# Kernel optimization log

Measured on AMD Instinct MI355X. Metric: run time of the kernel, lower is better.

## Reference

```python
import jax, jax.numpy as jnp
import numpy as np

B, S, P, D = 4, 2, 1024, 1024   # batch, sample_count, seq (== n_ctx), d_embed
I, H = 16, 64                   # n_heads, d_head
ALPHA = 1.0                     # weight_alpha


def setup_inputs() -> dict:
    key = jax.random.key(0)
    kx, kk, kq, kv, ko = jax.random.split(key, 5)
    scale = ALPHA / np.sqrt(D)
    return {
        "x": jax.random.normal(kx, (B, S, P, D), dtype=jnp.float32),
        "W_K": (scale * jax.random.normal(kk, (S, I, H, D))).astype(jnp.float32),
        "W_Q": (scale * jax.random.normal(kq, (S, I, H, D))).astype(jnp.float32),
        "W_V": (scale * jax.random.normal(kv, (S, I, H, D))).astype(jnp.float32),
        "W_O": (scale * jax.random.normal(ko, (S, D, I * H))).astype(jnp.float32),
    }


def reference(x, W_K, W_Q, W_V, W_O):
    # x: [b, s, p, d]; W_{K,Q,V}: [s, i, h, d]; W_O: [s, d, i*h]
    k = jnp.einsum('sihd,bspd->bsiph', W_K, x)
    q = jnp.einsum('sihd,bspd->bsiph', W_Q, x)
    v = jnp.einsum('sihd,bspd->bsiph', W_V, x)
    # scores: [b, s, i, q, p] (query rows, key cols)
    scores = jnp.einsum('bsiph,bsiqh->bsiqp', k, q)
    p = x.shape[-2]
    mask = jnp.tril(jnp.ones((p, p), dtype=x.dtype))  # causal lower-triangular
    # faithful to torch: tril(scores) - 1e10 * (1 - mask), scaled AFTER masking
    masked = scores * mask - 1.0e10 * (1.0 - mask)
    attn = jax.nn.softmax(masked / np.sqrt(H), axis=-1)
    z = jnp.einsum('bsiph,bsiqp->bsiqh', v, attn)      # [b, s, i, q, h]
    b = x.shape[0]
    z_flat = jnp.transpose(z, (0, 1, 3, 2, 4)).reshape(b, S, p, I * H)  # b s q (i h)
    out = jnp.einsum('sdf,bsqf->bsqd', W_O, z_flat)
    return out
```

## Files before the change

kernel.cpp:

```cpp
#include <hip/hip_runtime.h>
#include <hip/hip_bf16.h>
#include <cmath>

#define C_B 4
#define C_S 2
#define C_P 1024
#define C_D 1024
#define C_I 16
#define C_H 64

typedef unsigned short u16;
typedef unsigned int u32;
typedef __attribute__((ext_vector_type(8))) short short8;
typedef __attribute__((ext_vector_type(8))) __bf16 bf16x8;
typedef __attribute__((ext_vector_type(4))) float f32x4;
typedef __attribute__((ext_vector_type(16))) float f32x16;
typedef __attribute__((ext_vector_type(4))) u32 u32x4;

__device__ __forceinline__ u16 f2bf(float f) {
  union { float f; unsigned u; } c; c.f = f;
  unsigned u = c.u;
  u += 0x7fffu + ((u >> 16) & 1u);
  return (u16)(u >> 16);
}

__device__ __forceinline__ u32 cvtpk_bf16(float lo, float hi) {
  u32 r;
  asm("v_cvt_pk_bf16_f32 %0, %1, %2" : "=v"(r) : "v"(lo), "v"(hi));
  return r;
}

__device__ __forceinline__ float fexp2(float x) {
  return __builtin_amdgcn_exp2f(x);
}

__device__ __forceinline__ f32x16 mfma32(short8 a, short8 b, f32x16 c) {
  return __builtin_amdgcn_mfma_f32_32x32x16_bf16(
      __builtin_bit_cast(bf16x8, a), __builtin_bit_cast(bf16x8, b), c, 0, 0, 0);
}

__device__ __forceinline__ void load_lds16(const u16* g, u16* l) {
  __builtin_amdgcn_global_load_lds(
      (const __attribute__((address_space(1))) void*)g,
      (__attribute__((address_space(3))) void*)l, 16, 0, 0);
}

__global__ void cvt_all(const float* __restrict__ x,
                        const float* __restrict__ wq, const float* __restrict__ wk,
                        const float* __restrict__ wvp, const float* __restrict__ wo,
                        u16* __restrict__ xbf, u16* __restrict__ wall,
                        u16* __restrict__ wob) {
  const int b = blockIdx.x;
  if (b < 2048) {
    int i = b * 256 + threadIdx.x;
    const int n4 = (C_B * C_S * C_P * C_D) / 4, stride = 2048 * 256;
    for (; i < n4; i += stride) {
      float4 v = reinterpret_cast<const float4*>(x)[i];
      ushort4 o;
      o.x = f2bf(v.x); o.y = f2bf(v.y); o.z = f2bf(v.z); o.w = f2bf(v.w);
      reinterpret_cast<ushort4*>(xbf)[i] = o;
    }
  } else {
    const int j = b - 2048;
    const int t = j >> 9;
    const float* src = (t == 0) ? wq : (t == 1) ? wk : (t == 2) ? wvp : wo;
    int i = (j & 511) * 256 + threadIdx.x;
    const int stride = 512 * 256;
    for (; i < 524288; i += stride) {
      float4 v = reinterpret_cast<const float4*>(src)[i];
      ushort4 o;
      o.x = f2bf(v.x); o.y = f2bf(v.y); o.z = f2bf(v.z); o.w = f2bf(v.w);
      if (t < 3) {
        int s = i >> 18;
        int rem = i & 262143;
        reinterpret_cast<ushort4*>(wall)[s * 786432 + t * 262144 + rem] = o;
      } else {
        reinterpret_cast<ushort4*>(wob)[i] = o;
      }
    }
  }
}

template<int MODE>
__global__ __launch_bounds__(512, 2)
void gemm_bt(const u16* __restrict__ A, const u16* __restrict__ Bm, void* __restrict__ C) {
  __shared__ __align__(16) u16 lds[49152];
  const int tid = threadIdx.x;
  const int lane = tid & 63;
  const int wv = tid >> 6;
  const int wr = wv >> 2, wc = wv & 3;
  const int l31 = lane & 31, l5 = lane >> 5;

  const int h = (int)blockIdx.x;
  const int lid = (MODE == 3) ? ((h & 7) * 96 + (h >> 3)) : ((h & 7) * 32 + (h >> 3));
  const int bs  = (MODE == 3) ? (lid / 96) : (lid >> 5);
  const int r2  = (MODE == 3) ? (lid % 96) : (lid & 31);
  const int bx = r2 & 7, by = r2 >> 3;
  const int m0 = bx * 128, n0 = by * 256;

  const u16* Ab = A + (size_t)bs * (C_P * C_D);
  const u16* Bb = Bm + (size_t)(bs & 1) * (MODE == 3 ? 3 * 1048576 : 1048576);
  f32x16 acc[2][2] = {};

#define STAGE(T, BUF)                                                           \
  {                                                                             \
    const int kof = (T) * 64;                                                   \
    _Pragma("unroll")                                                           \
    for (int i = 0; i < 6; ++i) {                                               \
      int cid = tid + i * 512;                                                  \
      if (i < 2) {                                                              \
        int row = cid >> 3, c8 = (cid & 7) ^ (row & 7);                         \
        load_lds16(Ab + (size_t)(m0 + row) * 1024 + kof + c8 * 8,               \
                   lds + (BUF) * 8192 + cid * 8);                               \
      } else {                                                                  \
        int c2 = cid - 1024;                                                    \
        int row = c2 >> 3, c8 = (c2 & 7) ^ (row & 7);                           \
        load_lds16(Bb + (size_t)(n0 + row) * 1024 + kof + c8 * 8,               \
                   lds + 16384 + (BUF) * 16384 + c2 * 8);                       \
      }                                                                         \
    }                                                                           \
  }

  STAGE(0, 0)

  for (int t = 0; t < 16; ++t) {
    const int bbuf = t & 1;
    __builtin_amdgcn_s_barrier();
    if (t < 15) {
      STAGE(t + 1, bbuf ^ 1)
      asm volatile("s_waitcnt vmcnt(6)" ::: "memory");
    } else {
      asm volatile("s_waitcnt vmcnt(0)" ::: "memory");
    }
    __builtin_amdgcn_s_barrier();

    const u16* Ael = lds + bbuf * 8192;
    const u16* Bel = lds + 16384 + bbuf * 16384;
#pragma unroll
    for (int ks = 0; ks < 4; ++ks) {
      short8 am[2], bn[2];
#pragma unroll
      for (int mw = 0; mw < 2; ++mw) {
        int row = wr * 64 + mw * 32 + l31;
        int ch = (ks * 2 + l5) ^ (row & 7);
        am[mw] = *reinterpret_cast<const short8*>(Ael + row * 64 + ch * 8);
      }
#pragma unroll
      for (int nw = 0; nw < 2; ++nw) {
        int row = wc * 64 + nw * 32 + l31;
        int ch = (ks * 2 + l5) ^ (row & 7);
        bn[nw] = *reinterpret_cast<const short8*>(Bel + row * 64 + ch * 8);
      }
      __builtin_amdgcn_s_setprio(1);
#pragma unroll
      for (int mw = 0; mw < 2; ++mw)
#pragma unroll
        for (int nw = 0; nw < 2; ++nw)
          acc[mw][nw] = mfma32(am[mw], bn[nw], acc[mw][nw]);
      __builtin_amdgcn_s_setprio(0);
    }
  }
#undef STAGE

  if (MODE == 2) {
    float* dst = (float*)C + (size_t)bs * (C_P * C_D);
#pragma unroll
    for (int mw = 0; mw < 2; ++mw)
#pragma unroll
      for (int nw = 0; nw < 2; ++nw)
#pragma unroll
        for (int r = 0; r < 16; ++r) {
          int p = m0 + wr * 64 + mw * 32 + (r & 3) + 8 * (r >> 2) + 4 * l5;
          int col = n0 + wc * 64 + nw * 32 + l31;
          dst[(size_t)p * C_D + col] = acc[mw][nw][r];
        }
  } else {
    const int t3 = by >> 2;
    if (t3 < 2) {
      u16* dst = (u16*)C + (size_t)t3 * 8388608;
      const float scl = (t3 == 0) ? 0.18033688f : 1.0f;
#pragma unroll
      for (int mw = 0; mw < 2; ++mw)
#pragma unroll
        for (int nw = 0; nw < 2; ++nw)
#pragma unroll
          for (int r = 0; r < 16; ++r) {
            int p = m0 + wr * 64 + mw * 32 + (r & 3) + 8 * (r >> 2) + 4 * l5;
            int cg = (by & 3) * 256 + wc * 64 + nw * 32 + l31;
            dst[(size_t)(bs * C_I + (cg >> 6)) * 65536 + (size_t)p * C_H + (cg & 63)] =
                f2bf(acc[mw][nw][r] * scl);
          }
    } else {
      __syncthreads();
      char* trc = (char*)lds;
#pragma unroll
      for (int mw = 0; mw < 2; ++mw)
#pragma unroll
        for (int nw = 0; nw < 2; ++nw) {
          int nl = wc * 64 + nw * 32 + l31;
#pragma unroll
          for (int r = 0; r < 16; r += 2) {
            int pl = wr * 64 + mw * 32 + (r & 3) + 8 * (r >> 2) + 4 * l5;
            int pl2 = pl * 2;
            u32 wpk = cvtpk_bf16(acc[mw][nw][r], acc[mw][nw][r + 1]);
            *reinterpret_cast<u32*>(
                trc + nl * 256 + ((((pl2 >> 4) ^ (nl & 15)) << 4) | (pl2 & 15))) = wpk;
          }
        }
      __syncthreads();
      const int nl = tid >> 1, seg = tid & 1;
      const int cg = (by & 3) * 256 + nl;
      u16* dst = (u16*)C + 2 * 8388608 +
                 (size_t)(bs * C_I + (cg >> 6)) * 65536 + (size_t)(cg & 63) * C_P + m0;
#pragma unroll
      for (int j = 0; j < 8; ++j) {
        int c = seg * 8 + j;
        short8 v = *reinterpret_cast<const short8*>(
            trc + nl * 256 + ((c ^ (nl & 15)) << 4));
        *reinterpret_cast<short8*>(dst + c * 8) = v;
      }
    }
  }
}

__global__ __launch_bounds__(256, 4)
void attn_kernel(const u16* __restrict__ Q, const u16* __restrict__ K,
                 const u16* __restrict__ VT, u16* __restrict__ Z) {
  __shared__ __align__(16) u16 Kt[2][64 * 64];
  __shared__ __align__(16) u16 Vt[2][64 * 64];
  const int tid = threadIdx.x;
  const int lane = tid & 63, wv = tid >> 6;
  const int l31 = lane & 31, l5 = lane >> 5;
  const int b = (int)blockIdx.x;
  const int head = (b & 7) * 16 + ((b >> 3) & 15);
  const int y = b >> 7;
  const int qg = 7 - (y ^ (((y + 2) >> 2) & 1));
  const int bs = head >> 4, ih = head & 15;
  const int q0w = qg * 128 + wv * 32;
  const u16* Qh = Q + (size_t)head * (C_P * C_H);
  const u16* Kh = K + (size_t)head * (C_P * C_H);
  const u16* Vh = VT + (size_t)head * (C_P * C_H);
  const int ntiles = 2 * qg + 2;
  const int myq = q0w + l31;
  const int swz = (l31 & 7) << 4;

  short8 qf[4];
#pragma unroll
  for (int hk = 0; hk < 4; ++hk)
    qf[hk] = *reinterpret_cast<const short8*>(
        &Qh[(size_t)(q0w + l31) * C_H + hk * 16 + l5 * 8]);

  f32x16 zacc[2] = {};
  float mrun = -INFINITY, lrun = 0.f;

#define ASTAGE(t, buf)                                                          \
  {                                                                             \
    _Pragma("unroll")                                                           \
    for (int i = 0; i < 2; ++i) {                                               \
      int cid = wv * 128 + i * 64 + lane;                                       \
      int r = cid >> 3;                                                         \
      int sc = (cid & 7) ^ (r & 7);                                             \
      load_lds16(Kh + (size_t)((t) * 64 + r) * C_H + sc * 8, &Kt[buf][cid * 8]);\
      load_lds16(Vh + (size_t)r * C_P + (t) * 64 + sc * 8, &Vt[buf][cid * 8]);  \
    }                                                                           \
  }

  ASTAGE(0, 0)

  for (int t = 0; t < ntiles; ++t) {
    const int cur = t & 1;
    __builtin_amdgcn_s_barrier();
    if (t + 1 < ntiles) {
      ASTAGE(t + 1, cur ^ 1)
      asm volatile("s_waitcnt vmcnt(4)" ::: "memory");
    } else {
      asm volatile("s_waitcnt vmcnt(0)" ::: "memory");
    }
    __builtin_amdgcn_s_barrier();

    if (t * 64 <= q0w + 31) {
      const char* Kc = (const char*)Kt[cur];
      f32x16 sA[2];
      __builtin_amdgcn_s_setprio(1);
#pragma unroll
      for (int kt2 = 0; kt2 < 2; ++kt2) {
        f32x16 acc = {};
        int rb = (kt2 * 32 + l31) * 128 + ((l5 * 16) ^ swz);
#pragma unroll
        for (int hk = 0; hk < 4; ++hk) {
          short8 kf = *reinterpret_cast<const short8*>(Kc + (rb ^ (hk * 32)));
          acc = mfma32(kf, qf[hk], acc);
        }
        sA[kt2] = acc;
      }
      __builtin_amdgcn_s_setprio(0);

      if (t * 64 + 63 > q0w) {
#pragma unroll
        for (int kt2 = 0; kt2 < 2; ++kt2)
#pragma unroll
          for (int r = 0; r < 16; ++r) {
            int kv = t * 64 + kt2 * 32 + (r & 3) + 8 * (r >> 2) + 4 * l5;
            if (kv > myq) sA[kt2][r] = -1.8033688e9f;
          }
      }

      float tmax = sA[0][0];
#pragma unroll
      for (int r = 1; r < 16; ++r) tmax = fmaxf(tmax, sA[0][r]);
#pragma unroll
      for (int r = 0; r < 16; ++r) tmax = fmaxf(tmax, sA[1][r]);
      tmax = fmaxf(tmax, __shfl_xor(tmax, 32, 64));
      if (!__all(tmax - mrun <= 11.5416f)) {
        float mnew = fmaxf(mrun, tmax);
        float scal = fexp2(mrun - mnew);
        mrun = mnew;
        lrun *= scal;
#pragma unroll
        for (int r = 0; r < 16; ++r) {
          float sc = __shfl(scal, (r & 3) + 8 * (r >> 2) + 4 * l5, 64);
          zacc[0][r] *= sc;
          zacc[1][r] *= sc;
        }
      }
      float rsum = 0.f;
#pragma unroll
      for (int kt2 = 0; kt2 < 2; ++kt2)
#pragma unroll
        for (int r = 0; r < 16; ++r) {
          float e = fexp2(sA[kt2][r] - mrun);
          sA[kt2][r] = e;
          rsum += e;
        }
      rsum += __shfl_xor(rsum, 32, 64);
      lrun += rsum;

      short8 pa[4];
#pragma unroll
      for (int kt2 = 0; kt2 < 2; ++kt2) {
        u32 W[8];
#pragma unroll
        for (int i2 = 0; i2 < 8; ++i2)
          W[i2] = cvtpk_bf16(sA[kt2][2 * i2], sA[kt2][2 * i2 + 1]);
#pragma unroll
        for (int pr = 0; pr < 4; ++pr) {
          const int a = (pr & 1) + (pr >> 1) * 4;
          const int b2 = a + 2;
          u32 send = l5 ? W[a] : W[b2];
          u32 recv = __shfl_xor(send, 32, 64);
          u32 na = l5 ? recv : W[a];
          u32 nb = l5 ? W[b2] : recv;
          W[a] = na; W[b2] = nb;
        }
        u32x4 f0 = {W[0], W[1], W[2], W[3]};
        u32x4 f1 = {W[4], W[5], W[6], W[7]};
        pa[kt2 * 2 + 0] = __builtin_bit_cast(short8, f0);
        pa[kt2 * 2 + 1] = __builtin_bit_cast(short8, f1);
      }

      const char* Vc = (const char*)Vt[cur];
      __builtin_amdgcn_s_setprio(1);
#pragma unroll
      for (int kt = 0; kt < 4; ++kt)
#pragma unroll
        for (int ht = 0; ht < 2; ++ht) {
          int row = ht * 32 + l31;
          int vb = row * 128 + (((kt * 32) | (l5 * 16)) ^ ((row & 7) << 4));
          short8 vf = *reinterpret_cast<const short8*>(Vc + vb);
          zacc[ht] = mfma32(pa[kt], vf, zacc[ht]);
        }
      __builtin_amdgcn_s_setprio(0);
    }
  }

  float inv = 1.0f / lrun;
  u16* Zb = Z + (size_t)bs * (C_P * C_I * C_H) + ih * C_H;
#pragma unroll
  for (int r = 0; r < 16; ++r) {
    int qloc = (r & 3) + 8 * (r >> 2) + 4 * l5;
    float iv = __shfl(inv, qloc, 64);
    size_t rowo = (size_t)(q0w + qloc) * (C_I * C_H);
    Zb[rowo + l31]      = f2bf(zacc[0][r] * iv);
    Zb[rowo + 32 + l31] = f2bf(zacc[1][r] * iv);
  }
#undef ASTAGE
}

extern "C" void kernel_launch(void* const* d_in, const int* in_sizes, int n_in,
                              void* d_out, int out_size, void* d_ws, size_t ws_size,
                              hipStream_t stream) {
  const float* x  = (const float*)d_in[0];
  const float* wk = (const float*)d_in[1];
  const float* wq = (const float*)d_in[2];
  const float* wv = (const float*)d_in[3];
  const float* wo = (const float*)d_in[4];

  char* w = (char*)d_ws;
  u16* xbf  = (u16*)w;
  u16* wall = (u16*)(w + 16777216);
  u16* wob  = (u16*)(w + 29360128);
  u16* qws  = (u16*)(w + 33554432);
  u16* zws  = xbf;
  u16* kws  = qws + 8388608;
  u16* vtw  = kws + 8388608;

  cvt_all<<<4096, 256, 0, stream>>>(x, wq, wk, wv, wo, xbf, wall, wob);

  gemm_bt<3><<<768, 512, 0, stream>>>(xbf, wall, qws);

  attn_kernel<<<1024, 256, 0, stream>>>(qws, kws, vtw, zws);

  gemm_bt<2><<<256, 512, 0, stream>>>(zws, wob, d_out);
}
```

Measured before the change: 139.3 us.

## Single-buffer GEMM LDS with fragment-ordered layout to double occupancy

The GEMM kernel drops LDS double buffering, halving shared memory to 64 KB, and raises launch bounds from 2 to 4 blocks per CU. The LDS layout becomes MFMA-fragment-ordered, so each lane reads a contiguous 16 bytes and the XOR swizzle goes away. Global loads for the next tile are now issued only after compute and fully awaited before the next compute, so load latency is exposed within a block. The bet is that more resident blocks hide that latency, but the launch bounds may force register spills.

```diff
diff --git a/kernel.cpp b/kernel.cpp
--- a/kernel.cpp
+++ b/kernel.cpp
@@ -82,9 +82,9 @@
 }
 
 template<int MODE>
-__global__ __launch_bounds__(512, 2)
+__global__ __launch_bounds__(512, 4)
 void gemm_bt(const u16* __restrict__ A, const u16* __restrict__ Bm, void* __restrict__ C) {
-  __shared__ __align__(16) u16 lds[49152];
+  __shared__ __align__(16) u16 lds[32768];
   const int tid = threadIdx.x;
   const int lane = tid & 63;
   const int wv = tid >> 6;
@@ -102,55 +102,44 @@
   const u16* Bb = Bm + (size_t)(bs & 1) * (MODE == 3 ? 3 * 1048576 : 1048576);
   f32x16 acc[2][2] = {};
 
-#define STAGE(T, BUF)                                                           \
+#define STAGE(T)                                                                \
   {                                                                             \
     const int kof = (T) * 64;                                                   \
     _Pragma("unroll")                                                           \
     for (int i = 0; i < 6; ++i) {                                               \
-      int cid = tid + i * 512;                                                  \
+      int o = tid + i * 512;                                                    \
       if (i < 2) {                                                              \
-        int row = cid >> 3, c8 = (cid & 7) ^ (row & 7);                         \
-        load_lds16(Ab + (size_t)(m0 + row) * 1024 + kof + c8 * 8,               \
-                   lds + (BUF) * 8192 + cid * 8);                               \
+        int f = o >> 6, w = o & 63;                                             \
+        int row = (f >> 2) * 32 + (w & 31);                                     \
+        int kc = (f & 3) * 2 + (w >> 5);                                        \
+        load_lds16(Ab + (size_t)(m0 + row) * 1024 + kof + kc * 8, lds + o * 8); \
       } else {                                                                  \
-        int c2 = cid - 1024;                                                    \
-        int row = c2 >> 3, c8 = (c2 & 7) ^ (row & 7);                           \
-        load_lds16(Bb + (size_t)(n0 + row) * 1024 + kof + c8 * 8,               \
-                   lds + 16384 + (BUF) * 16384 + c2 * 8);                       \
+        int o2 = o - 1024;                                                      \
+        int f = o2 >> 6, w = o2 & 63;                                           \
+        int row = (f >> 2) * 32 + (w & 31);                                     \
+        int kc = (f & 3) * 2 + (w >> 5);                                        \
+        load_lds16(Bb + (size_t)(n0 + row) * 1024 + kof + kc * 8,               \
+                   lds + 8192 + o2 * 8);                                        \
       }                                                                         \
     }                                                                           \
   }
 
-  STAGE(0, 0)
+  STAGE(0)
 
   for (int t = 0; t < 16; ++t) {
-    const int bbuf = t & 1;
+    asm volatile("s_waitcnt vmcnt(0)" ::: "memory");
     __builtin_amdgcn_s_barrier();
-    if (t < 15) {
-      STAGE(t + 1, bbuf ^ 1)
-      asm volatile("s_waitcnt vmcnt(6)" ::: "memory");
-    } else {
-      asm volatile("s_waitcnt vmcnt(0)" ::: "memory");
-    }
-    __builtin_amdgcn_s_barrier();
-
-    const u16* Ael = lds + bbuf * 8192;
-    const u16* Bel = lds + 16384 + bbuf * 16384;
 #pragma unroll
     for (int ks = 0; ks < 4; ++ks) {
       short8 am[2], bn[2];
 #pragma unroll
-      for (int mw = 0; mw < 2; ++mw) {
-        int row = wr * 64 + mw * 32 + l31;
-        int ch = (ks * 2 + l5) ^ (row & 7);
-        am[mw] = *reinterpret_cast<const short8*>(Ael + row * 64 + ch * 8);
-      }
-#pragma unroll
-      for (int nw = 0; nw < 2; ++nw) {
-        int row = wc * 64 + nw * 32 + l31;
-        int ch = (ks * 2 + l5) ^ (row & 7);
-        bn[nw] = *reinterpret_cast<const short8*>(Bel + row * 64 + ch * 8);
-      }
+      for (int mw = 0; mw < 2; ++mw)
+        am[mw] = *reinterpret_cast<const short8*>(
+            lds + ((wr * 2 + mw) * 4 + ks) * 512 + lane * 8);
+#pragma unroll
+      for (int nw = 0; nw < 2; ++nw)
+        bn[nw] = *reinterpret_cast<const short8*>(
+            lds + 8192 + ((wc * 2 + nw) * 4 + ks) * 512 + lane * 8);
       __builtin_amdgcn_s_setprio(1);
 #pragma unroll
       for (int mw = 0; mw < 2; ++mw)
@@ -159,6 +148,8 @@
           acc[mw][nw] = mfma32(am[mw], bn[nw], acc[mw][nw]);
       __builtin_amdgcn_s_setprio(0);
     }
+    __builtin_amdgcn_s_barrier();
+    if (t < 15) STAGE(t + 1)
   }
 #undef STAGE
 
```

New measurement: 191.0 us. 37.1% more time.
